# Kernel optimization log

Measured on AMD Instinct MI355X. Metric: run time of the kernel, lower is better.

## Reference

```python
import jax, jax.numpy as jnp
import numpy as np

N, D_IN, D_BLOCK, D_OUT, E, K = 65536, 128, 256, 128, 8, 2


def setup_inputs() -> dict:
    key = jax.random.key(0)
    ks = jax.random.split(key, 8)
    s_in = 1.0 / np.sqrt(D_IN)
    s_h = 1.0 / np.sqrt(D_BLOCK)
    return {
        "x": jax.random.normal(ks[0], (N, D_IN), jnp.float32),
        "Wg": jax.random.normal(ks[1], (D_IN, E), jnp.float32) * s_in,
        "W1": jax.random.normal(ks[2], (E, D_IN, D_BLOCK), jnp.float32) * s_in,
        "b1": jax.random.normal(ks[3], (E, D_BLOCK), jnp.float32) * 0.01,
        "W2": jax.random.normal(ks[4], (E, D_BLOCK, D_BLOCK), jnp.float32) * s_h,
        "b2": jax.random.normal(ks[5], (E, D_BLOCK), jnp.float32) * 0.01,
        "Wo": jax.random.normal(ks[6], (D_BLOCK, D_OUT), jnp.float32) * s_h,
        "bo": jax.random.normal(ks[7], (D_OUT,), jnp.float32) * 0.01,
    }


def reference(x, Wg, W1, b1, W2, b2, Wo, bo):
    # Router: linear gate -> top-k -> softmax over the k selected logits,
    # scattered back to a dense [N, E] combine-weight matrix (zeros elsewhere).
    logits = x @ Wg                                   # [N, E]
    topv, topi = jax.lax.top_k(logits, K)             # [N, K]
    w_topk = jax.nn.softmax(topv, axis=-1)            # [N, K]
    onehot = jax.nn.one_hot(topi, E, dtype=x.dtype)   # [N, K, E]
    weights = jnp.einsum("nk,nke->ne", w_topk, onehot)  # [N, E]

    # Expert MLPs (n_blocks=2, ReLU, dropout=0 at eval), computed for all
    # experts over all tokens; unselected experts have weight 0, so the
    # weighted combine reproduces the original masked gather/scatter math.
    h = jax.nn.relu(jnp.einsum("nd,edh->enh", x, W1) + b1[:, None, :])   # [E,N,H]
    h = jax.nn.relu(jnp.einsum("enh,ehg->eng", h, W2) + b2[:, None, :])  # [E,N,H]
    y = jnp.einsum("enh,ho->eno", h, Wo) + bo                             # [E,N,O]

    # Weighted scatter-add combine: outs[n] = sum_e weights[n,e] * y[e,n]
    return jnp.einsum("ne,eno->no", weights, y)
```

## Files before the change

### kernel.cpp

```cpp
#include <hip/hip_runtime.h>
#include <math.h>

typedef unsigned short ushort_t;
typedef __attribute__((ext_vector_type(8))) short bf16x8;
typedef __attribute__((ext_vector_type(4))) float f32x4;
typedef __attribute__((ext_vector_type(8))) unsigned short u16x8;
typedef __attribute__((ext_vector_type(2))) unsigned int u32x2;
typedef __attribute__((ext_vector_type(4))) unsigned int u32x4;

#define N_TOK 65536
#define DIN 128
#define HD 256
#define DOUT 128
#define NEXP 8
#define MT 64
#define MAX_TILES (N_TOK / MT)

__device__ __forceinline__ unsigned short f2bf(float f) {
    union { float f; unsigned int i; } v; v.f = f;
    unsigned int i = v.i;
    return (unsigned short)((i + 0x7FFFu + ((i >> 16) & 1u)) >> 16);
}

#define RT_BLOCK 1024
#define RT_TPB 128

__global__ __launch_bounds__(RT_BLOCK)
void router_kernel(const float* __restrict__ x,
                   const float* __restrict__ Wg,
                   const float* __restrict__ W1,
                   const float* __restrict__ W2,
                   const float* __restrict__ Wo,
                   const float* __restrict__ bo,
                   int* __restrict__ counts,
                   int* __restrict__ list_tok,
                   float* __restrict__ list_w,
                   ushort_t* __restrict__ wt1f,
                   ushort_t* __restrict__ wt2f,
                   ushort_t* __restrict__ wotf,
                   float* __restrict__ out) {
    __shared__ float wgsT[NEXP * 132];
    __shared__ int lcnt[NEXP];
    __shared__ int lbase[NEXP];
    int tid = threadIdx.x;
    if (tid < NEXP) lcnt[tid] = 0;
    if (tid < DIN * NEXP) {
        int ee = tid & 7, k = tid >> 3;
        wgsT[ee * 132 + k] = Wg[tid];
    }
    {
        const float4* bo4 = (const float4*)bo;
        float4* ob = (float4*)(out + (size_t)blockIdx.x * RT_TPB * DOUT);
#pragma unroll
        for (int i = 0; i < 4; i++) {
            int idx = i * RT_BLOCK + tid;
            ob[idx] = bo4[idx & 31];
        }
    }
    if (blockIdx.x < 100) {
        int id = blockIdx.x * RT_BLOCK + tid;
        const float* src; ushort_t* dst; int Nn, ksteps, c;
        if (id < 32768) {
            int ee = id >> 12; c = id & 4095;
            Nn = HD; ksteps = 4; src = W1 + (size_t)ee * DIN * HD; dst = wt1f + (size_t)id * 8;
        } else if (id < 98304) {
            int t = id - 32768; int ee = t >> 13; c = t & 8191;
            Nn = HD; ksteps = 8; src = W2 + (size_t)ee * HD * HD; dst = wt2f + (size_t)t * 8;
        } else {
            int t = id - 98304; c = t;
            Nn = DOUT; ksteps = 8; src = Wo; dst = wotf + (size_t)t * 8;
        }
        int L = c & 63; int kc = c >> 6;
        int kstep = kc % ksteps; int ntile = kc / ksteps;
        int qq = L >> 4, mm = L & 15;
        int n = ntile * 16 + mm; int k0 = kstep * 32 + qq * 8;
        u16x8 v;
#pragma unroll
        for (int j = 0; j < 8; j++) v[j] = f2bf(src[(size_t)(k0 + j) * Nn + n]);
        *(u16x8*)dst = v;
    }
    __syncthreads();

    int e = tid & 7;
    int tl = tid >> 3;
    int n = blockIdx.x * RT_TPB + tl;
    const float4* xr = (const float4*)(x + (size_t)n * DIN);
    const float4* wv4 = (const float4*)(wgsT + e * 132);
    float lg = 0.f;
#pragma unroll 8
    for (int kk = 0; kk < 32; kk++) {
        float4 xv = xr[kk];
        float4 wv = wv4[kk];
        lg += xv.x * wv.x;
        lg += xv.y * wv.y;
        lg += xv.z * wv.z;
        lg += xv.w * wv.w;
    }
    float v0 = lg; int e0 = e;
#pragma unroll
    for (int d = 1; d < 8; d <<= 1) {
        float ov = __shfl_xor(v0, d, 64);
        int oe = __shfl_xor(e0, d, 64);
        if (ov > v0 || (ov == v0 && oe < e0)) { v0 = ov; e0 = oe; }
    }
    float mv = (e == e0) ? -3.0e38f : lg;
    float v1 = mv; int e1 = e;
#pragma unroll
    for (int d = 1; d < 8; d <<= 1) {
        float ov = __shfl_xor(v1, d, 64);
        int oe = __shfl_xor(e1, d, 64);
        if (ov > v1 || (ov == v1 && oe < e1)) { v1 = ov; e1 = oe; }
    }
    float t = expf(v1 - v0);
    float inv = 1.0f / (1.0f + t);
    float w0 = inv, w1 = t * inv;

    bool writer = (e == 0);
    int p0 = 0, p1 = 0;
    if (writer) {
        p0 = atomicAdd(&lcnt[e0], 1);
        p1 = atomicAdd(&lcnt[e1], 1);
    }
    __syncthreads();
    if (tid < NEXP) lbase[tid] = atomicAdd(&counts[tid * 32], lcnt[tid]);
    __syncthreads();
    if (writer) {
        int q0 = lbase[e0] + p0;
        list_tok[e0 * N_TOK + q0] = n;
        list_w[e0 * N_TOK + q0] = w0;
        int q1 = lbase[e1] + p1;
        list_tok[e1 * N_TOK + q1] = n;
        list_w[e1 * N_TOK + q1] = w1;
    }
}

__global__ __launch_bounds__(256, 3)
void expert_kernel(const float* __restrict__ x,
                   const int* __restrict__ counts,
                   const int* __restrict__ list_tok,
                   const float* __restrict__ list_w,
                   const ushort_t* __restrict__ wt1f,
                   const ushort_t* __restrict__ wt2f,
                   const ushort_t* __restrict__ wotf,
                   const float* __restrict__ b1,
                   const float* __restrict__ b2,
                   float* __restrict__ out) {
    int e = blockIdx.x & 7;
    int tile = blockIdx.x >> 3;
    int cnt = counts[e * 32];
    int base = tile * MT;
    if (base >= cnt) return;
    int rows = cnt - base; if (rows > MT) rows = MT;

    __shared__ __align__(16) ushort_t bufH[16384];
    __shared__ int toks_s[MT];
    __shared__ float wts_s[MT];

    int tid = threadIdx.x;
    int lane = tid & 63;
    int w = tid >> 6;
    int q = lane >> 4;
    int mcol = lane & 15;

    const bf16x8* W1A = (const bf16x8*)(wt1f + (size_t)e * 4096 * 8);
    const bf16x8* W2A = (const bf16x8*)(wt2f + (size_t)e * 8192 * 8);
    const bf16x8* WoB = (const bf16x8*)wotf;
    const bf16x8* Hlbs = (const bf16x8*)bufH;

    if (tid < MT) {
        int rr = tid < rows ? tid : rows - 1;
        toks_s[tid] = list_tok[(size_t)e * N_TOK + base + rr];
        wts_s[tid] = list_w[(size_t)e * N_TOK + base + rr];
    }

    bf16x8 a1r[2][4];
#pragma unroll
    for (int rtl = 0; rtl < 4; rtl++)
        a1r[0][rtl] = W1A[((w * 4 + rtl) * 4 + 0) * 64 + lane];

    {
        int row = tid & 63;
        int rr = row < rows ? row : rows - 1;
        int tok = list_tok[(size_t)e * N_TOK + base + rr];
        const float* xrow = x + (size_t)tok * DIN;
#pragma unroll
        for (int i = 0; i < 4; i++) {
            int kchunk = (tid >> 6) + i * 4;
            const float4* src = (const float4*)(xrow + kchunk * 8);
            float4 lo = src[0], hi = src[1];
            unsigned p0, p1, p2, p3;
            asm("v_cvt_pk_bf16_f32 %0, %1, %2" : "=v"(p0) : "v"(lo.x), "v"(lo.y));
            asm("v_cvt_pk_bf16_f32 %0, %1, %2" : "=v"(p1) : "v"(lo.z), "v"(lo.w));
            asm("v_cvt_pk_bf16_f32 %0, %1, %2" : "=v"(p2) : "v"(hi.x), "v"(hi.y));
            asm("v_cvt_pk_bf16_f32 %0, %1, %2" : "=v"(p3) : "v"(hi.z), "v"(hi.w));
            int dchunk = (i * 4 + (row >> 4)) * 64 + (kchunk & 3) * 16 + (row & 15);
            u32x4 v; v.x = p0; v.y = p1; v.z = p2; v.w = p3;
            *(u32x4*)(&bufH[dchunk * 8]) = v;
        }
    }
    __syncthreads();

    f32x4 acc[4][4];
#pragma unroll
    for (int rtl = 0; rtl < 4; rtl++)
#pragma unroll
        for (int ct = 0; ct < 4; ct++) acc[rtl][ct] = (f32x4){0.f, 0.f, 0.f, 0.f};
#pragma unroll
    for (int ks = 0; ks < 4; ks++) {
        const int cur = ks & 1, nxt = cur ^ 1;
        if (ks < 3) {
#pragma unroll
            for (int rtl = 0; rtl < 4; rtl++)
                a1r[nxt][rtl] = W1A[((w * 4 + rtl) * 4 + ks + 1) * 64 + lane];
        }
        bf16x8 bf_[4];
#pragma unroll
        for (int ct = 0; ct < 4; ct++) bf_[ct] = Hlbs[(ks * 4 + ct) * 64 + lane];
#pragma unroll
        for (int rtl = 0; rtl < 4; rtl++)
#pragma unroll
            for (int ct = 0; ct < 4; ct++)
                acc[rtl][ct] = __builtin_amdgcn_mfma_f32_16x16x32_bf16(a1r[cur][rtl], bf_[ct], acc[rtl][ct], 0, 0, 0);
    }
    bf16x8 a2r[2][4];
#pragma unroll
    for (int rtl = 0; rtl < 4; rtl++)
        a2r[0][rtl] = W2A[((w * 4 + rtl) * 8 + 0) * 64 + lane];

    float4 b1v[4];
#pragma unroll
    for (int rtl = 0; rtl < 4; rtl++)
        b1v[rtl] = *(const float4*)(b1 + e * HD + w * 64 + rtl * 16 + q * 4);

    __syncthreads();

#pragma unroll
    for (int rtl = 0; rtl < 4; rtl++) {
        int ks2 = w * 2 + (rtl >> 1);
        int q2 = (rtl * 2 + (q >> 1)) & 3;
        int uoff = (ks2 * 4 * 64 + q2 * 16 + mcol) * 8 + (q & 1) * 4;
#pragma unroll
        for (int ct = 0; ct < 4; ct++) {
            float v0 = acc[rtl][ct][0] + b1v[rtl].x; v0 = v0 > 0.f ? v0 : 0.f;
            float v1 = acc[rtl][ct][1] + b1v[rtl].y; v1 = v1 > 0.f ? v1 : 0.f;
            float v2 = acc[rtl][ct][2] + b1v[rtl].z; v2 = v2 > 0.f ? v2 : 0.f;
            float v3 = acc[rtl][ct][3] + b1v[rtl].w; v3 = v3 > 0.f ? v3 : 0.f;
            unsigned d0, d1;
            asm("v_cvt_pk_bf16_f32 %0, %1, %2" : "=v"(d0) : "v"(v0), "v"(v1));
            asm("v_cvt_pk_bf16_f32 %0, %1, %2" : "=v"(d1) : "v"(v2), "v"(v3));
            u32x2 dd; dd.x = d0; dd.y = d1;
            *(u32x2*)(&bufH[uoff + ct * 512]) = dd;
        }
    }
    __syncthreads();

    f32x4 acc2[4][4];
#pragma unroll
    for (int rtl = 0; rtl < 4; rtl++)
#pragma unroll
        for (int ct = 0; ct < 4; ct++) acc2[rtl][ct] = (f32x4){0.f, 0.f, 0.f, 0.f};
#pragma unroll
    for (int ks = 0; ks < 8; ks++) {
        const int cur = ks & 1, nxt = cur ^ 1;
        if (ks < 7) {
#pragma unroll
            for (int rtl = 0; rtl < 4; rtl++)
                a2r[nxt][rtl] = W2A[((w * 4 + rtl) * 8 + ks + 1) * 64 + lane];
        }
        bf16x8 bf_[4];
#pragma unroll
        for (int ct = 0; ct < 4; ct++) bf_[ct] = Hlbs[(ks * 4 + ct) * 64 + lane];
#pragma unroll
        for (int rtl = 0; rtl < 4; rtl++)
#pragma unroll
            for (int ct = 0; ct < 4; ct++)
                acc2[rtl][ct] = __builtin_amdgcn_mfma_f32_16x16x32_bf16(a2r[cur][rtl], bf_[ct], acc2[rtl][ct], 0, 0, 0);
    }
    bf16x8 b3r[2][2];
#pragma unroll
    for (int nt = 0; nt < 2; nt++)
        b3r[0][nt] = WoB[((w * 2 + nt) * 8 + 0) * 64 + lane];

    float4 b2v[4];
#pragma unroll
    for (int rtl = 0; rtl < 4; rtl++)
        b2v[rtl] = *(const float4*)(b2 + e * HD + w * 64 + rtl * 16 + q * 4);

    __syncthreads();

#pragma unroll
    for (int rtl = 0; rtl < 4; rtl++) {
        int ks2 = w * 2 + (rtl >> 1);
        int q2 = (rtl * 2 + (q >> 1)) & 3;
        int uoff = (ks2 * 4 * 64 + q2 * 16 + mcol) * 8 + (q & 1) * 4;
#pragma unroll
        for (int ct = 0; ct < 4; ct++) {
            float v0 = acc2[rtl][ct][0] + b2v[rtl].x; v0 = v0 > 0.f ? v0 : 0.f;
            float v1 = acc2[rtl][ct][1] + b2v[rtl].y; v1 = v1 > 0.f ? v1 : 0.f;
            float v2 = acc2[rtl][ct][2] + b2v[rtl].z; v2 = v2 > 0.f ? v2 : 0.f;
            float v3 = acc2[rtl][ct][3] + b2v[rtl].w; v3 = v3 > 0.f ? v3 : 0.f;
            unsigned d0, d1;
            asm("v_cvt_pk_bf16_f32 %0, %1, %2" : "=v"(d0) : "v"(v0), "v"(v1));
            asm("v_cvt_pk_bf16_f32 %0, %1, %2" : "=v"(d1) : "v"(v2), "v"(v3));
            u32x2 dd; dd.x = d0; dd.y = d1;
            *(u32x2*)(&bufH[uoff + ct * 512]) = dd;
        }
    }
    __syncthreads();

    f32x4 acc3[4][2];
#pragma unroll
    for (int mt = 0; mt < 4; mt++)
#pragma unroll
        for (int nt = 0; nt < 2; nt++) acc3[mt][nt] = (f32x4){0.f, 0.f, 0.f, 0.f};
#pragma unroll
    for (int ks = 0; ks < 8; ks++) {
        const int cur = ks & 1, nxt = cur ^ 1;
        if (ks < 7) {
#pragma unroll
            for (int nt = 0; nt < 2; nt++)
                b3r[nxt][nt] = WoB[((w * 2 + nt) * 8 + ks + 1) * 64 + lane];
        }
        bf16x8 af_[4];
#pragma unroll
        for (int mt = 0; mt < 4; mt++) af_[mt] = Hlbs[(ks * 4 + mt) * 64 + lane];
#pragma unroll
        for (int nt = 0; nt < 2; nt++)
#pragma unroll
            for (int mt = 0; mt < 4; mt++)
                acc3[mt][nt] = __builtin_amdgcn_mfma_f32_16x16x32_bf16(af_[mt], b3r[cur][nt], acc3[mt][nt], 0, 0, 0);
    }
#pragma unroll
    for (int mt = 0; mt < 4; mt++) {
#pragma unroll
        for (int r = 0; r < 4; r++) {
            int row = mt * 16 + q * 4 + r;
            if (row < rows) {
                int tok = toks_s[row];
                float wgt = wts_s[row];
                float* dst = out + (size_t)tok * DOUT;
#pragma unroll
                for (int nt = 0; nt < 2; nt++) {
                    int col = (w * 2 + nt) * 16 + mcol;
                    atomicAdd(&dst[col], wgt * acc3[mt][nt][r]);
                }
            }
        }
    }
}

extern "C" void kernel_launch(void* const* d_in, const int* in_sizes, int n_in,
                              void* d_out, int out_size, void* d_ws, size_t ws_size,
                              hipStream_t stream) {
    const float* x  = (const float*)d_in[0];
    const float* Wg = (const float*)d_in[1];
    const float* W1 = (const float*)d_in[2];
    const float* b1 = (const float*)d_in[3];
    const float* W2 = (const float*)d_in[4];
    const float* b2 = (const float*)d_in[5];
    const float* Wo = (const float*)d_in[6];
    const float* bo = (const float*)d_in[7];
    float* out = (float*)d_out;

    char* ws = (char*)d_ws;
    size_t off = 0;
    int* counts    = (int*)(ws + off);    off += 1024;
    int* list_tok  = (int*)(ws + off);    off += (size_t)NEXP * N_TOK * 4;
    float* list_w  = (float*)(ws + off);  off += (size_t)NEXP * N_TOK * 4;
    ushort_t* wt1f = (ushort_t*)(ws + off); off += (size_t)NEXP * DIN * HD * 2;
    ushort_t* wt2f = (ushort_t*)(ws + off); off += (size_t)NEXP * HD * HD * 2;
    ushort_t* wotf = (ushort_t*)(ws + off); off += (size_t)HD * DOUT * 2;

    hipMemsetAsync(counts, 0, 1024, stream);
    router_kernel<<<N_TOK / RT_TPB, RT_BLOCK, 0, stream>>>(
        x, Wg, W1, W2, Wo, bo, counts, list_tok, list_w, wt1f, wt2f, wotf, out);
    expert_kernel<<<NEXP * MAX_TILES, 256, 0, stream>>>(x, counts, list_tok, list_w,
                                                        wt1f, wt2f, wotf, b1, b2, out);
}
```

Before: 197.8 us.

## Swizzle LDS layout, coalesce x gather, fold output bias into carrier atomics

Applies an XOR swizzle to every LDS access in the expert kernel to reduce bank conflicts on the bf16 fragment reads and writes. Rewrites the x-tile gather so consecutive threads read consecutive 32-byte chunks of the same token row. Removes the bias initialisation of the output from the router kernel: the output is now zeroed with a memset, and the first expert of each token adds bo inside its atomic add, flagged by storing a negated routing weight. This trades a full output write in the router for a memset plus one extra per-element bias load in the atomic epilogue.

```diff
diff --git a/kernel.cpp b/kernel.cpp
--- a/kernel.cpp
+++ b/kernel.cpp
@@ -31,14 +31,12 @@
                    const float* __restrict__ W1,
                    const float* __restrict__ W2,
                    const float* __restrict__ Wo,
-                   const float* __restrict__ bo,
                    int* __restrict__ counts,
                    int* __restrict__ list_tok,
                    float* __restrict__ list_w,
                    ushort_t* __restrict__ wt1f,
                    ushort_t* __restrict__ wt2f,
-                   ushort_t* __restrict__ wotf,
-                   float* __restrict__ out) {
+                   ushort_t* __restrict__ wotf) {
     __shared__ float wgsT[NEXP * 132];
     __shared__ int lcnt[NEXP];
     __shared__ int lbase[NEXP];
@@ -47,15 +45,6 @@
     if (tid < DIN * NEXP) {
         int ee = tid & 7, k = tid >> 3;
         wgsT[ee * 132 + k] = Wg[tid];
-    }
-    {
-        const float4* bo4 = (const float4*)bo;
-        float4* ob = (float4*)(out + (size_t)blockIdx.x * RT_TPB * DOUT);
-#pragma unroll
-        for (int i = 0; i < 4; i++) {
-            int idx = i * RT_BLOCK + tid;
-            ob[idx] = bo4[idx & 31];
-        }
     }
     if (blockIdx.x < 100) {
         int id = blockIdx.x * RT_BLOCK + tid;
@@ -127,12 +116,14 @@
     if (writer) {
         int q0 = lbase[e0] + p0;
         list_tok[e0 * N_TOK + q0] = n;
-        list_w[e0 * N_TOK + q0] = w0;
+        list_w[e0 * N_TOK + q0] = -w0;
         int q1 = lbase[e1] + p1;
         list_tok[e1 * N_TOK + q1] = n;
         list_w[e1 * N_TOK + q1] = w1;
     }
 }
+
+#define LDSA(c) ((char*)bufH + ((((c) << 4) ^ ((((c) >> 4) & 3) << 4) ^ ((((c) >> 8) & 3) << 6))))
 
 __global__ __launch_bounds__(256, 3)
 void expert_kernel(const float* __restrict__ x,
@@ -144,6 +135,7 @@
                    const ushort_t* __restrict__ wotf,
                    const float* __restrict__ b1,
                    const float* __restrict__ b2,
+                   const float* __restrict__ bo,
                    float* __restrict__ out) {
     int e = blockIdx.x & 7;
     int tile = blockIdx.x >> 3;
@@ -165,7 +157,6 @@
     const bf16x8* W1A = (const bf16x8*)(wt1f + (size_t)e * 4096 * 8);
     const bf16x8* W2A = (const bf16x8*)(wt2f + (size_t)e * 8192 * 8);
     const bf16x8* WoB = (const bf16x8*)wotf;
-    const bf16x8* Hlbs = (const bf16x8*)bufH;
 
     if (tid < MT) {
         int rr = tid < rows ? tid : rows - 1;
@@ -178,25 +169,21 @@
     for (int rtl = 0; rtl < 4; rtl++)
         a1r[0][rtl] = W1A[((w * 4 + rtl) * 4 + 0) * 64 + lane];
 
-    {
-        int row = tid & 63;
+    for (int c = tid; c < 1024; c += 256) {
+        int row = c >> 4;
+        int kchunk = c & 15;
         int rr = row < rows ? row : rows - 1;
         int tok = list_tok[(size_t)e * N_TOK + base + rr];
-        const float* xrow = x + (size_t)tok * DIN;
-#pragma unroll
-        for (int i = 0; i < 4; i++) {
-            int kchunk = (tid >> 6) + i * 4;
-            const float4* src = (const float4*)(xrow + kchunk * 8);
-            float4 lo = src[0], hi = src[1];
-            unsigned p0, p1, p2, p3;
-            asm("v_cvt_pk_bf16_f32 %0, %1, %2" : "=v"(p0) : "v"(lo.x), "v"(lo.y));
-            asm("v_cvt_pk_bf16_f32 %0, %1, %2" : "=v"(p1) : "v"(lo.z), "v"(lo.w));
-            asm("v_cvt_pk_bf16_f32 %0, %1, %2" : "=v"(p2) : "v"(hi.x), "v"(hi.y));
-            asm("v_cvt_pk_bf16_f32 %0, %1, %2" : "=v"(p3) : "v"(hi.z), "v"(hi.w));
-            int dchunk = (i * 4 + (row >> 4)) * 64 + (kchunk & 3) * 16 + (row & 15);
-            u32x4 v; v.x = p0; v.y = p1; v.z = p2; v.w = p3;
-            *(u32x4*)(&bufH[dchunk * 8]) = v;
-        }
+        const float4* src = (const float4*)(x + (size_t)tok * DIN + kchunk * 8);
+        float4 lo = src[0], hi = src[1];
+        unsigned p0, p1, p2, p3;
+        asm("v_cvt_pk_bf16_f32 %0, %1, %2" : "=v"(p0) : "v"(lo.x), "v"(lo.y));
+        asm("v_cvt_pk_bf16_f32 %0, %1, %2" : "=v"(p1) : "v"(lo.z), "v"(lo.w));
+        asm("v_cvt_pk_bf16_f32 %0, %1, %2" : "=v"(p2) : "v"(hi.x), "v"(hi.y));
+        asm("v_cvt_pk_bf16_f32 %0, %1, %2" : "=v"(p3) : "v"(hi.z), "v"(hi.w));
+        int dchunk = ((kchunk >> 2) * 4 + (row >> 4)) * 64 + (kchunk & 3) * 16 + (row & 15);
+        u32x4 v; v.x = p0; v.y = p1; v.z = p2; v.w = p3;
+        *(u32x4*)LDSA(dchunk) = v;
     }
     __syncthreads();
 
@@ -215,7 +202,7 @@
         }
         bf16x8 bf_[4];
 #pragma unroll
-        for (int ct = 0; ct < 4; ct++) bf_[ct] = Hlbs[(ks * 4 + ct) * 64 + lane];
+        for (int ct = 0; ct < 4; ct++) bf_[ct] = *(const bf16x8*)LDSA((ks * 4 + ct) * 64 + lane);
 #pragma unroll
         for (int rtl = 0; rtl < 4; rtl++)
 #pragma unroll
@@ -238,7 +225,7 @@
     for (int rtl = 0; rtl < 4; rtl++) {
         int ks2 = w * 2 + (rtl >> 1);
         int q2 = (rtl * 2 + (q >> 1)) & 3;
-        int uoff = (ks2 * 4 * 64 + q2 * 16 + mcol) * 8 + (q & 1) * 4;
+        int chunk0 = ks2 * 256 + q2 * 16 + mcol;
 #pragma unroll
         for (int ct = 0; ct < 4; ct++) {
             float v0 = acc[rtl][ct][0] + b1v[rtl].x; v0 = v0 > 0.f ? v0 : 0.f;
@@ -249,7 +236,7 @@
             asm("v_cvt_pk_bf16_f32 %0, %1, %2" : "=v"(d0) : "v"(v0), "v"(v1));
             asm("v_cvt_pk_bf16_f32 %0, %1, %2" : "=v"(d1) : "v"(v2), "v"(v3));
             u32x2 dd; dd.x = d0; dd.y = d1;
-            *(u32x2*)(&bufH[uoff + ct * 512]) = dd;
+            *(u32x2*)(LDSA(chunk0 + ct * 64) + (q & 1) * 8) = dd;
         }
     }
     __syncthreads();
@@ -269,7 +256,7 @@
         }
         bf16x8 bf_[4];
 #pragma unroll
-        for (int ct = 0; ct < 4; ct++) bf_[ct] = Hlbs[(ks * 4 + ct) * 64 + lane];
+        for (int ct = 0; ct < 4; ct++) bf_[ct] = *(const bf16x8*)LDSA((ks * 4 + ct) * 64 + lane);
 #pragma unroll
         for (int rtl = 0; rtl < 4; rtl++)
 #pragma unroll
@@ -292,7 +279,7 @@
     for (int rtl = 0; rtl < 4; rtl++) {
         int ks2 = w * 2 + (rtl >> 1);
         int q2 = (rtl * 2 + (q >> 1)) & 3;
-        int uoff = (ks2 * 4 * 64 + q2 * 16 + mcol) * 8 + (q & 1) * 4;
+        int chunk0 = ks2 * 256 + q2 * 16 + mcol;
 #pragma unroll
         for (int ct = 0; ct < 4; ct++) {
             float v0 = acc2[rtl][ct][0] + b2v[rtl].x; v0 = v0 > 0.f ? v0 : 0.f;
@@ -303,7 +290,7 @@
             asm("v_cvt_pk_bf16_f32 %0, %1, %2" : "=v"(d0) : "v"(v0), "v"(v1));
             asm("v_cvt_pk_bf16_f32 %0, %1, %2" : "=v"(d1) : "v"(v2), "v"(v3));
             u32x2 dd; dd.x = d0; dd.y = d1;
-            *(u32x2*)(&bufH[uoff + ct * 512]) = dd;
+            *(u32x2*)(LDSA(chunk0 + ct * 64) + (q & 1) * 8) = dd;
         }
     }
     __syncthreads();
@@ -323,7 +310,7 @@
         }
         bf16x8 af_[4];
 #pragma unroll
-        for (int mt = 0; mt < 4; mt++) af_[mt] = Hlbs[(ks * 4 + mt) * 64 + lane];
+        for (int mt = 0; mt < 4; mt++) af_[mt] = *(const bf16x8*)LDSA((ks * 4 + mt) * 64 + lane);
 #pragma unroll
         for (int nt = 0; nt < 2; nt++)
 #pragma unroll
@@ -337,12 +324,15 @@
             int row = mt * 16 + q * 4 + r;
             if (row < rows) {
                 int tok = toks_s[row];
-                float wgt = wts_s[row];
+                float wraw = wts_s[row];
+                float wgt = fabsf(wraw);
+                bool carrier = wraw < 0.f;
                 float* dst = out + (size_t)tok * DOUT;
 #pragma unroll
                 for (int nt = 0; nt < 2; nt++) {
                     int col = (w * 2 + nt) * 16 + mcol;
-                    atomicAdd(&dst[col], wgt * acc3[mt][nt][r]);
+                    float addv = wgt * acc3[mt][nt][r] + (carrier ? bo[col] : 0.f);
+                    atomicAdd(&dst[col], addv);
                 }
             }
         }
@@ -372,8 +362,9 @@
     ushort_t* wotf = (ushort_t*)(ws + off); off += (size_t)HD * DOUT * 2;
 
     hipMemsetAsync(counts, 0, 1024, stream);
+    hipMemsetAsync(out, 0, (size_t)N_TOK * DOUT * 4, stream);
     router_kernel<<<N_TOK / RT_TPB, RT_BLOCK, 0, stream>>>(
-        x, Wg, W1, W2, Wo, bo, counts, list_tok, list_w, wt1f, wt2f, wotf, out);
+        x, Wg, W1, W2, Wo, counts, list_tok, list_w, wt1f, wt2f, wotf);
     expert_kernel<<<NEXP * MAX_TILES, 256, 0, stream>>>(x, counts, list_tok, list_w,
-                                                        wt1f, wt2f, wotf, b1, b2, out);
+                                                        wt1f, wt2f, wotf, b1, b2, bo, out);
 }
```

After: 222.9 us. +12.6%, slower.
